# Kernel tuning notes

Measured on AMD Instinct MI355X. Metric: run time of the kernel, lower is better.

## Reference

```python
import jax, jax.numpy as jnp
import numpy as np
import math

D_EMB = 1024
N_HEADS = 16
SCALE = 0.02
B, T = 4, 2048


def _norm(x):
    # torch.std_mean default: unbiased std (ddof=1) over last dim
    m = jnp.mean(x, axis=-1, keepdims=True)
    s = jnp.std(x, axis=-1, keepdims=True, ddof=1)
    return (x - m) / (s + 1e-05)


def setup_inputs() -> dict:
    key = jax.random.key(0)
    kx, kw = jax.random.split(key)
    x = jax.random.normal(kx, (B, D_EMB, T), dtype=jnp.float32)
    qkv = jax.random.normal(kw, (3, N_HEADS, D_EMB, D_EMB // N_HEADS), dtype=jnp.float32) * SCALE
    return {"x": x, "qkv": qkv}


def reference(x, qkv):
    Bsz, D, Tlen = x.shape
    H = qkv.shape[1]
    # (3, B, H, T, d_head)
    h = jnp.einsum('bdt,nhde->nbhte', x, qkv)
    q, k, v = h[0], h[1], h[2]
    q = _norm(q)
    k = _norm(k)
    scale = math.sqrt(D // H)  # torch: sqrt(d_emb // H)
    attn = jnp.einsum('bhte,bhse->bhts', q, k) / scale  # [B,H,T,T]
    attn = jax.nn.softmax(attn, axis=-1)
    out = jnp.einsum('bhts,bhse->bhet', attn, v)  # [B,H,d_head,T]
    return out.reshape(Bsz, D, Tlen)
```

## Files before the change

### kernel.cpp

```cpp
#include <hip/hip_runtime.h>
#include <hip/hip_bf16.h>

#define B_SZ 4
#define NHEADS 16
#define T_SZ 2048
#define DE 1024
#define DH 64
#define BH (B_SZ*NHEADS)
#define SCL 0.18033688011112042f

typedef __attribute__((ext_vector_type(8))) short short8;
typedef __attribute__((ext_vector_type(4))) float float4v;
typedef __attribute__((ext_vector_type(16))) float f32x16;
typedef __attribute__((ext_vector_type(2))) unsigned int uint2v;
typedef __attribute__((ext_vector_type(4))) unsigned int uint4v;

__device__ __forceinline__ short f2bf(float f) {
    __hip_bfloat16 h = __float2bfloat16(f);
    return *reinterpret_cast<short*>(&h);
}
__device__ __forceinline__ unsigned int pack_bf2(float a, float b) {
    float2 f; f.x = a; f.y = b;
    __hip_bfloat162 h = __float22bfloat162_rn(f);
    return *reinterpret_cast<unsigned int*>(&h);
}
__device__ __forceinline__ float4v zero4() {
    float4v z = {0.f, 0.f, 0.f, 0.f};
    return z;
}
__device__ __forceinline__ int swz(int row, int g) {
    return row * 64 + (((g) ^ (row & 7)) << 3);
}
__device__ __forceinline__ void gl_lds16(const short* g, short* l) {
    __builtin_amdgcn_global_load_lds(
        (const __attribute__((address_space(1))) void*)g,
        (__attribute__((address_space(3))) void*)l, 16, 0, 0);
}

__global__ __launch_bounds__(256) void transpose_k(const float* __restrict__ src,
                                                   short* __restrict__ dst,
                                                   int R, int C) {
    __shared__ __align__(16) short tile[64 * 65];
    int c0 = blockIdx.x * 64, r0 = blockIdx.y * 64;
    src += (size_t)blockIdx.z * R * C;
    dst += (size_t)blockIdx.z * R * C;
    int tid = threadIdx.x;
#pragma unroll
    for (int it = 0; it < 16; ++it) {
        int idx = it * 256 + tid;
        int rr = idx >> 6, cc = idx & 63;
        tile[cc * 65 + rr] = f2bf(src[(size_t)(r0 + rr) * C + c0 + cc]);
    }
    __syncthreads();
#pragma unroll
    for (int it = 0; it < 16; ++it) {
        int idx = it * 256 + tid;
        int cc = idx >> 6, rr = idx & 63;
        dst[(size_t)(c0 + cc) * R + r0 + rr] = tile[cc * 65 + rr];
    }
}

__global__ __launch_bounds__(256, 2) void qkv_k(const short* __restrict__ XT,
                                                const short* __restrict__ WT,
                                                short* __restrict__ Qw,
                                                short* __restrict__ Kw,
                                                short* __restrict__ Vt) {
    __shared__ __align__(16) short ldsA[2][128 * 64];
    __shared__ __align__(16) short ldsB[2][128 * 64];
    int b  = blockIdx.x >> 4;
    int t0 = (blockIdx.x & 15) * 128;
    int n  = blockIdx.y >> 3;
    int h0 = (blockIdx.y & 7) * 2;
    int tid = threadIdx.x, wave = tid >> 6, lane = tid & 63;
    int l15 = lane & 15, quad = lane >> 4;
    int wr = wave >> 1, wc = wave & 1;

    const short* Arow = XT + ((size_t)b * T_SZ + t0) * DE;
    const short* Brow = WT + ((size_t)n * 1024 + h0 * 64) * DE;

    int rA = lane >> 3;
    int gl = (lane & 7) ^ rA;

    float4v acc[4][4];
#pragma unroll
    for (int mm = 0; mm < 4; ++mm)
#pragma unroll
        for (int j = 0; j < 4; ++j) acc[mm][j] = zero4();

    auto STAGE = [&](short* La, short* Lb, int k0) {
#pragma unroll
        for (int it = 0; it < 4; ++it) {
            int rowbase = it * 32 + wave * 8;
            gl_lds16(&Arow[(size_t)(rowbase + rA) * DE + k0 + gl * 8],
                     &La[(it * 256 + wave * 64) * 8]);
            gl_lds16(&Brow[(size_t)(rowbase + rA) * DE + k0 + gl * 8],
                     &Lb[(it * 256 + wave * 64) * 8]);
        }
    };
    auto COMPUTE = [&](const short* La, const short* Lb) {
#pragma unroll
        for (int ks = 0; ks < 2; ++ks) {
            short8 af[4], bf[4];
#pragma unroll
            for (int mm = 0; mm < 4; ++mm)
                af[mm] = *(const short8*)&La[swz(64 * wr + 16 * mm + l15, 4 * ks + quad)];
#pragma unroll
            for (int j = 0; j < 4; ++j)
                bf[j] = *(const short8*)&Lb[swz(64 * wc + 16 * j + l15, 4 * ks + quad)];
#pragma unroll
            for (int mm = 0; mm < 4; ++mm)
#pragma unroll
                for (int j = 0; j < 4; ++j)
                    acc[mm][j] = __builtin_amdgcn_mfma_f32_16x16x32_bf16(af[mm], bf[j], acc[mm][j], 0, 0, 0);
        }
    };

    STAGE(ldsA[0], ldsB[0], 0);
    __syncthreads();
    for (int k0 = 0; k0 < DE; k0 += 128) {
        STAGE(ldsA[1], ldsB[1], k0 + 64);
        COMPUTE(ldsA[0], ldsB[0]);
        __syncthreads();
        if (k0 + 128 < DE)
            STAGE(ldsA[0], ldsB[0], k0 + 128);
        COMPUTE(ldsA[1], ldsB[1]);
        __syncthreads();
    }

    int h = h0 + wc;
    int bh = b * NHEADS + h;
#pragma unroll
    for (int mm = 0; mm < 4; ++mm) {
        int tbase = t0 + 64 * wr + 16 * mm;
        if (n < 2) {
            float oscale = (n == 0) ? SCL : 1.0f;
            float mu[4], inv[4];
#pragma unroll
            for (int r = 0; r < 4; ++r) {
                float s1 = 0.f, s2 = 0.f;
#pragma unroll
                for (int jj = 0; jj < 4; ++jj) {
                    float v = acc[mm][jj][r];
                    s1 += v; s2 += v * v;
                }
                for (int sh = 1; sh < 16; sh <<= 1) {
                    s1 += __shfl_xor(s1, sh, 64);
                    s2 += __shfl_xor(s2, sh, 64);
                }
                mu[r] = s1 * (1.0f / 64.0f);
                float var = (s2 - 64.0f * mu[r] * mu[r]) * (1.0f / 63.0f);
                var = fmaxf(var, 0.0f);
                inv[r] = oscale / (sqrtf(var) + 1e-5f);
            }
            short* dst = (n == 0 ? Qw : Kw) + (size_t)bh * T_SZ * DH;
#pragma unroll
            for (int r = 0; r < 4; ++r) {
                int t = tbase + quad * 4 + r;
#pragma unroll
                for (int jj = 0; jj < 4; ++jj) {
                    float v = (acc[mm][jj][r] - mu[r]) * inv[r];
                    dst[(size_t)t * DH + 16 * jj + l15] = f2bf(v);
                }
            }
        } else {
#pragma unroll
            for (int r = 0; r < 4; ++r) {
                int t = tbase + quad * 4 + r;
#pragma unroll
                for (int jj = 0; jj < 4; ++jj) {
                    Vt[((size_t)bh * DH + 16 * jj + l15) * T_SZ + t] =
                        f2bf(acc[mm][jj][r]);
                }
            }
        }
    }
}

__global__ __launch_bounds__(256, 2) void attn_k(const short* __restrict__ Qw,
                                                 const short* __restrict__ Kw,
                                                 const short* __restrict__ Vt,
                                                 float* __restrict__ out) {
    __shared__ __align__(16) char smem[32768];
    short* ldsK = (short*)smem;
    short* ldsV = (short*)(smem + 16384);
    float* ldsL = (float*)smem;

    int bh = blockIdx.x;
    int t0 = blockIdx.y * 256;
    int b = bh >> 4, h = bh & 15;
    int tid = threadIdx.x, wave = tid >> 6, lane = tid & 63;
    int l31 = lane & 31, b5 = lane >> 5;
    int tw = t0 + 64 * wave;

    const short* Qp = Qw + (size_t)bh * T_SZ * DH;
    const short* Kp = Kw + (size_t)bh * T_SZ * DH;
    const short* Vp = Vt + (size_t)bh * DH * T_SZ;

    int rA = lane >> 3;
    int g8 = lane & 7;

    short8 qf[2][4];
#pragma unroll
    for (int tt = 0; tt < 2; ++tt)
#pragma unroll
        for (int kk = 0; kk < 4; ++kk)
            qf[tt][kk] = *(const short8*)&Qp[(size_t)(tw + 32 * tt + l31) * DH + 16 * kk + 8 * b5];

    f32x16 o[2][2];
    float ol[2] = {0.f, 0.f};
#pragma unroll
    for (int tt = 0; tt < 2; ++tt)
#pragma unroll
        for (int et = 0; et < 2; ++et) o[tt][et] = (f32x16)0.0f;

    short8 rk[2], rv[2];
    auto LOADNEXT = [&](int s) {
#pragma unroll
        for (int it = 0; it < 2; ++it) {
            int row = 16 * wave + 8 * it + rA;
            rk[it] = *(const short8*)&Kp[(size_t)(s + row) * DH + g8 * 8];
            rv[it] = *(const short8*)&Vp[(size_t)row * T_SZ + s + g8 * 8];
        }
    };
    auto WRITESTAGE = [&](int buf) {
        short* Kb = ldsK + buf * 4096;
        short* Vb = ldsV + buf * 4096;
#pragma unroll
        for (int it = 0; it < 2; ++it) {
            int row = 16 * wave + 8 * it + rA;
            *(short8*)&Kb[swz(row, g8)] = rk[it];
            *(short8*)&Vb[swz(row, g8)] = rv[it];
        }
    };

    LOADNEXT(0);
    WRITESTAGE(0);
    __syncthreads();

    for (int s0 = 0; s0 < T_SZ; s0 += 64) {
        int cur = (s0 >> 6) & 1;
        LOADNEXT((s0 + 64) & (T_SZ - 1));
        const short* Kc = ldsK + cur * 4096;
        const short* Vc = ldsV + cur * 4096;

        short8 af[2][4];
#pragma unroll
        for (int ss = 0; ss < 2; ++ss)
#pragma unroll
            for (int kk = 0; kk < 4; ++kk)
                af[ss][kk] = *(const short8*)&Kc[swz(32 * ss + l31, 2 * kk + b5)];

        uint2v u[2][2][4];
#pragma unroll
        for (int tt = 0; tt < 2; ++tt) {
#pragma unroll
            for (int ss = 0; ss < 2; ++ss) {
                f32x16 z = (f32x16)0.0f;
#pragma unroll
                for (int kk = 0; kk < 4; ++kk)
                    z = __builtin_amdgcn_mfma_f32_32x32x16_bf16(af[ss][kk], qf[tt][kk], z, 0, 0, 0);
#pragma unroll
                for (int g = 0; g < 4; ++g) {
                    float p0 = __builtin_amdgcn_exp2f(z[4 * g + 0]);
                    float p1 = __builtin_amdgcn_exp2f(z[4 * g + 1]);
                    float p2 = __builtin_amdgcn_exp2f(z[4 * g + 2]);
                    float p3 = __builtin_amdgcn_exp2f(z[4 * g + 3]);
                    ol[tt] += (p0 + p1) + (p2 + p3);
                    u[tt][ss][g].x = pack_bf2(p0, p1);
                    u[tt][ss][g].y = pack_bf2(p2, p3);
                }
            }
        }

        short8 vf[2][4];
#pragma unroll
        for (int et = 0; et < 2; ++et)
#pragma unroll
            for (int kk = 0; kk < 4; ++kk)
                vf[et][kk] = *(const short8*)&Vc[swz(32 * et + l31, 2 * kk + b5)];

#pragma unroll
        for (int tt = 0; tt < 2; ++tt) {
#pragma unroll
            for (int kks = 0; kks < 4; ++kks) {
                const int ssb = kks >> 1, ga = 2 * (kks & 1);
                unsigned a0 = u[tt][ssb][ga].x,     a1 = u[tt][ssb][ga].y;
                unsigned b0 = u[tt][ssb][ga + 1].x, b1 = u[tt][ssb][ga + 1].y;
                asm("v_permlane32_swap_b32 %0, %1" : "+v"(a0), "+v"(b0));
                asm("v_permlane32_swap_b32 %0, %1" : "+v"(a1), "+v"(b1));
                uint4v up; up.x = a0; up.y = a1; up.z = b0; up.w = b1;
                short8 pf = *(short8*)&up;
                o[tt][0] = __builtin_amdgcn_mfma_f32_32x32x16_bf16(pf, vf[0][kks], o[tt][0], 0, 0, 0);
                o[tt][1] = __builtin_amdgcn_mfma_f32_32x32x16_bf16(pf, vf[1][kks], o[tt][1], 0, 0, 0);
            }
        }

        WRITESTAGE(cur ^ 1);
        __syncthreads();
    }

#pragma unroll
    for (int tt = 0; tt < 2; ++tt) {
        float l = ol[tt] + __shfl_xor(ol[tt], 32, 64);
        if (lane < 32) ldsL[wave * 64 + tt * 32 + lane] = 1.0f / l;
    }

#pragma unroll
    for (int tt = 0; tt < 2; ++tt) {
#pragma unroll
        for (int g = 0; g < 4; ++g) {
            float4v ri = *(const float4v*)&ldsL[wave * 64 + tt * 32 + 8 * g + 4 * b5];
#pragma unroll
            for (int et = 0; et < 2; ++et) {
                float4v ov;
#pragma unroll
                for (int i = 0; i < 4; ++i) ov[i] = o[tt][et][4 * g + i] * ri[i];
                *(float4v*)&out[(size_t)(b * DE + h * DH + 32 * et + l31) * T_SZ
                                + tw + 32 * tt + 8 * g + 4 * b5] = ov;
            }
        }
    }
}

extern "C" void kernel_launch(void* const* d_in, const int* in_sizes, int n_in,
                              void* d_out, int out_size, void* d_ws, size_t ws_size,
                              hipStream_t stream) {
    const float* x = (const float*)d_in[0];
    const float* w = (const float*)d_in[1];
    float* out = (float*)d_out;
    char* ws = (char*)d_ws;

    const size_t XT_BYTES = (size_t)B_SZ * T_SZ * DE * 2;
    const size_t WT_BYTES = (size_t)3 * NHEADS * DH * DE * 2;
    const size_t QKV_BYTES = (size_t)BH * T_SZ * DH * 2;

    short* XT = (short*)(ws);
    short* WT = (short*)(ws + XT_BYTES);
    short* Qw = (short*)(ws + XT_BYTES + WT_BYTES);
    short* Kw = (short*)(ws + XT_BYTES + WT_BYTES + QKV_BYTES);
    short* Vt = (short*)(ws + XT_BYTES + WT_BYTES + 2 * QKV_BYTES);

    transpose_k<<<dim3(T_SZ / 64, DE / 64, B_SZ), 256, 0, stream>>>(x, XT, DE, T_SZ);
    transpose_k<<<dim3(1, DE / 64, 3 * NHEADS), 256, 0, stream>>>(w, WT, DE, DH);
    qkv_k<<<dim3(64, 24), 256, 0, stream>>>(XT, WT, Qw, Kw, Vt);
    attn_k<<<dim3(BH, T_SZ / 256), 256, 0, stream>>>(Qw, Kw, Vt, out);
}
```

Measured before the change: 237.4 us.

## Halve attention query tile per wave to raise occupancy and add setprio

Each wave of the attention kernel now processes 32 query rows instead of 64, so a block covers 128 queries and the grid doubles. Register use drops (one Q fragment set, two output accumulators), which allows launch bounds of 4 blocks per CU instead of 2. K and V fragments are now loaded from LDS just before each MFMA, and s_setprio brackets the compute section to favour MFMA issue. The trade-off is that every K/V tile staged in LDS is reused by half as many queries, so global and LDS traffic for K/V per query doubles.

After: 246.7 us. 3.9% more time.

```diff
diff --git a/kernel.cpp b/kernel.cpp
--- a/kernel.cpp
+++ b/kernel.cpp
@@ -176,7 +176,7 @@
     }
 }
 
-__global__ __launch_bounds__(256, 2) void attn_k(const short* __restrict__ Qw,
+__global__ __launch_bounds__(256, 4) void attn_k(const short* __restrict__ Qw,
                                                  const short* __restrict__ Kw,
                                                  const short* __restrict__ Vt,
                                                  float* __restrict__ out) {
@@ -186,11 +186,11 @@
     float* ldsL = (float*)smem;
 
     int bh = blockIdx.x;
-    int t0 = blockIdx.y * 256;
+    int t0 = blockIdx.y * 128;
     int b = bh >> 4, h = bh & 15;
     int tid = threadIdx.x, wave = tid >> 6, lane = tid & 63;
     int l31 = lane & 31, b5 = lane >> 5;
-    int tw = t0 + 64 * wave;
+    int tw = t0 + 32 * wave;
 
     const short* Qp = Qw + (size_t)bh * T_SZ * DH;
     const short* Kp = Kw + (size_t)bh * T_SZ * DH;
@@ -199,19 +199,13 @@
     int rA = lane >> 3;
     int g8 = lane & 7;
 
-    short8 qf[2][4];
-#pragma unroll
-    for (int tt = 0; tt < 2; ++tt)
-#pragma unroll
-        for (int kk = 0; kk < 4; ++kk)
-            qf[tt][kk] = *(const short8*)&Qp[(size_t)(tw + 32 * tt + l31) * DH + 16 * kk + 8 * b5];
-
-    f32x16 o[2][2];
-    float ol[2] = {0.f, 0.f};
-#pragma unroll
-    for (int tt = 0; tt < 2; ++tt)
-#pragma unroll
-        for (int et = 0; et < 2; ++et) o[tt][et] = (f32x16)0.0f;
+    short8 qf[4];
+#pragma unroll
+    for (int kk = 0; kk < 4; ++kk)
+        qf[kk] = *(const short8*)&Qp[(size_t)(tw + l31) * DH + 16 * kk + 8 * b5];
+
+    f32x16 o0 = (f32x16)0.0f, o1 = (f32x16)0.0f;
+    float ol = 0.f;
 
     short8 rk[2], rv[2];
     auto LOADNEXT = [&](int s) {
@@ -243,82 +237,67 @@
         const short* Kc = ldsK + cur * 4096;
         const short* Vc = ldsV + cur * 4096;
 
-        short8 af[2][4];
-#pragma unroll
-        for (int ss = 0; ss < 2; ++ss)
-#pragma unroll
-            for (int kk = 0; kk < 4; ++kk)
-                af[ss][kk] = *(const short8*)&Kc[swz(32 * ss + l31, 2 * kk + b5)];
-
-        uint2v u[2][2][4];
-#pragma unroll
-        for (int tt = 0; tt < 2; ++tt) {
-#pragma unroll
-            for (int ss = 0; ss < 2; ++ss) {
-                f32x16 z = (f32x16)0.0f;
-#pragma unroll
-                for (int kk = 0; kk < 4; ++kk)
-                    z = __builtin_amdgcn_mfma_f32_32x32x16_bf16(af[ss][kk], qf[tt][kk], z, 0, 0, 0);
-#pragma unroll
-                for (int g = 0; g < 4; ++g) {
-                    float p0 = __builtin_amdgcn_exp2f(z[4 * g + 0]);
-                    float p1 = __builtin_amdgcn_exp2f(z[4 * g + 1]);
-                    float p2 = __builtin_amdgcn_exp2f(z[4 * g + 2]);
-                    float p3 = __builtin_amdgcn_exp2f(z[4 * g + 3]);
-                    ol[tt] += (p0 + p1) + (p2 + p3);
-                    u[tt][ss][g].x = pack_bf2(p0, p1);
-                    u[tt][ss][g].y = pack_bf2(p2, p3);
-                }
-            }
-        }
-
-        short8 vf[2][4];
-#pragma unroll
-        for (int et = 0; et < 2; ++et)
-#pragma unroll
-            for (int kk = 0; kk < 4; ++kk)
-                vf[et][kk] = *(const short8*)&Vc[swz(32 * et + l31, 2 * kk + b5)];
-
-#pragma unroll
-        for (int tt = 0; tt < 2; ++tt) {
-#pragma unroll
-            for (int kks = 0; kks < 4; ++kks) {
-                const int ssb = kks >> 1, ga = 2 * (kks & 1);
-                unsigned a0 = u[tt][ssb][ga].x,     a1 = u[tt][ssb][ga].y;
-                unsigned b0 = u[tt][ssb][ga + 1].x, b1 = u[tt][ssb][ga + 1].y;
-                asm("v_permlane32_swap_b32 %0, %1" : "+v"(a0), "+v"(b0));
-                asm("v_permlane32_swap_b32 %0, %1" : "+v"(a1), "+v"(b1));
-                uint4v up; up.x = a0; up.y = a1; up.z = b0; up.w = b1;
-                short8 pf = *(short8*)&up;
-                o[tt][0] = __builtin_amdgcn_mfma_f32_32x32x16_bf16(pf, vf[0][kks], o[tt][0], 0, 0, 0);
-                o[tt][1] = __builtin_amdgcn_mfma_f32_32x32x16_bf16(pf, vf[1][kks], o[tt][1], 0, 0, 0);
-            }
-        }
+        __builtin_amdgcn_s_setprio(1);
+
+        uint2v u[2][4];
+#pragma unroll
+        for (int ss = 0; ss < 2; ++ss) {
+            f32x16 z = (f32x16)0.0f;
+#pragma unroll
+            for (int kk = 0; kk < 4; ++kk) {
+                short8 ak = *(const short8*)&Kc[swz(32 * ss + l31, 2 * kk + b5)];
+                z = __builtin_amdgcn_mfma_f32_32x32x16_bf16(ak, qf[kk], z, 0, 0, 0);
+            }
+#pragma unroll
+            for (int g = 0; g < 4; ++g) {
+                float p0 = __builtin_amdgcn_exp2f(z[4 * g + 0]);
+                float p1 = __builtin_amdgcn_exp2f(z[4 * g + 1]);
+                float p2 = __builtin_amdgcn_exp2f(z[4 * g + 2]);
+                float p3 = __builtin_amdgcn_exp2f(z[4 * g + 3]);
+                ol += (p0 + p1) + (p2 + p3);
+                u[ss][g].x = pack_bf2(p0, p1);
+                u[ss][g].y = pack_bf2(p2, p3);
+            }
+        }
+
+#pragma unroll
+        for (int kks = 0; kks < 4; ++kks) {
+            const int ssb = kks >> 1, ga = 2 * (kks & 1);
+            unsigned a0 = u[ssb][ga].x,     a1 = u[ssb][ga].y;
+            unsigned b0 = u[ssb][ga + 1].x, b1 = u[ssb][ga + 1].y;
+            asm("v_permlane32_swap_b32 %0, %1" : "+v"(a0), "+v"(b0));
+            asm("v_permlane32_swap_b32 %0, %1" : "+v"(a1), "+v"(b1));
+            uint4v up; up.x = a0; up.y = a1; up.z = b0; up.w = b1;
+            short8 pf = *(short8*)&up;
+            short8 v0 = *(const short8*)&Vc[swz(l31, 2 * kks + b5)];
+            short8 v1 = *(const short8*)&Vc[swz(32 + l31, 2 * kks + b5)];
+            o0 = __builtin_amdgcn_mfma_f32_32x32x16_bf16(pf, v0, o0, 0, 0, 0);
+            o1 = __builtin_amdgcn_mfma_f32_32x32x16_bf16(pf, v1, o1, 0, 0, 0);
+        }
+
+        __builtin_amdgcn_s_setprio(0);
 
         WRITESTAGE(cur ^ 1);
         __syncthreads();
     }
 
-#pragma unroll
-    for (int tt = 0; tt < 2; ++tt) {
-        float l = ol[tt] + __shfl_xor(ol[tt], 32, 64);
-        if (lane < 32) ldsL[wave * 64 + tt * 32 + lane] = 1.0f / l;
-    }
-
-#pragma unroll
-    for (int tt = 0; tt < 2; ++tt) {
-#pragma unroll
-        for (int g = 0; g < 4; ++g) {
-            float4v ri = *(const float4v*)&ldsL[wave * 64 + tt * 32 + 8 * g + 4 * b5];
-#pragma unroll
-            for (int et = 0; et < 2; ++et) {
-                float4v ov;
-#pragma unroll
-                for (int i = 0; i < 4; ++i) ov[i] = o[tt][et][4 * g + i] * ri[i];
-                *(float4v*)&out[(size_t)(b * DE + h * DH + 32 * et + l31) * T_SZ
-                                + tw + 32 * tt + 8 * g + 4 * b5] = ov;
-            }
-        }
+    {
+        float l = ol + __shfl_xor(ol, 32, 64);
+        if (lane < 32) ldsL[wave * 32 + lane] = 1.0f / l;
+    }
+
+#pragma unroll
+    for (int g = 0; g < 4; ++g) {
+        float4v ri = *(const float4v*)&ldsL[wave * 32 + 8 * g + 4 * b5];
+        float4v ov;
+#pragma unroll
+        for (int i = 0; i < 4; ++i) ov[i] = o0[4 * g + i] * ri[i];
+        *(float4v*)&out[(size_t)(b * DE + h * DH + l31) * T_SZ
+                        + tw + 8 * g + 4 * b5] = ov;
+#pragma unroll
+        for (int i = 0; i < 4; ++i) ov[i] = o1[4 * g + i] * ri[i];
+        *(float4v*)&out[(size_t)(b * DE + h * DH + 32 + l31) * T_SZ
+                        + tw + 8 * g + 4 * b5] = ov;
     }
 }
 
@@ -343,5 +322,5 @@
     transpose_k<<<dim3(T_SZ / 64, DE / 64, B_SZ), 256, 0, stream>>>(x, XT, DE, T_SZ);
     transpose_k<<<dim3(1, DE / 64, 3 * NHEADS), 256, 0, stream>>>(w, WT, DE, DH);
     qkv_k<<<dim3(64, 24), 256, 0, stream>>>(XT, WT, Qw, Kw, Vt);
-    attn_k<<<dim3(BH, T_SZ / 256), 256, 0, stream>>>(Qw, Kw, Vt, out);
-}
+    attn_k<<<dim3(BH, T_SZ / 128), 256, 0, stream>>>(Qw, Kw, Vt, out);
+}
```
